# Kernel tuning notes

Hardware: AMD Instinct MI355X
Metric: run time of the kernel (lower is better)

The kernel has to match this reference:

```python
import jax, jax.numpy as jnp
import numpy as np

B, S, T, E, H = 16, 96, 50, 128, 128
D2 = 2 * H
V = 32000
NGRAM = 2
ALPHA = 0.25


def _lstm(x, Wih, Whh, b, reverse=False):
    # x: [N, T, E] -> outputs [N, T, H], final h, c (PyTorch gate order i,f,g,o)
    xt = jnp.swapaxes(x, 0, 1)
    if reverse:
        xt = xt[::-1]
    n = x.shape[0]
    h = Whh.shape[1]
    init = (jnp.zeros((n, h), x.dtype), jnp.zeros((n, h), x.dtype))

    def step(carry, xin):
        hprev, cprev = carry
        g = xin @ Wih.T + hprev @ Whh.T + b
        i, f, gg, o = jnp.split(g, 4, axis=-1)
        c = jax.nn.sigmoid(f) * cprev + jax.nn.sigmoid(i) * jnp.tanh(gg)
        hnew = jax.nn.sigmoid(o) * jnp.tanh(c)
        return (hnew, c), hnew

    (hT, cT), outs = jax.lax.scan(step, init, xt)
    if reverse:
        outs = outs[::-1]
    return jnp.swapaxes(outs, 0, 1), hT, cT


def _gru(x, h, Wi, Wh, bi, bh):
    # PyTorch GRUCell, gate order r,z,n
    gi = x @ Wi.T + bi
    gh = h @ Wh.T + bh
    ir, iz, inn = jnp.split(gi, 3, axis=-1)
    hr, hz, hn = jnp.split(gh, 3, axis=-1)
    r = jax.nn.sigmoid(ir + hr)
    z = jax.nn.sigmoid(iz + hz)
    n = jnp.tanh(inn + r * hn)
    return (1.0 - z) * n + z * h


def _norm_scale(x):
    # (||x|| + alpha) / (||x|| + 1), detached as in the original
    v = jnp.linalg.norm(x, axis=1)
    return jax.lax.stop_gradient(((v + ALPHA) / (v + 1.0))[:, None])


def setup_inputs() -> dict:
    key = jax.random.key(0)
    ks = jax.random.split(key, 30)
    rn = lambda k, sh: jax.random.normal(k, sh, jnp.float32) * 0.05
    return {
        "enc_batch": jax.random.randint(ks[0], (B * S, T), 0, V),
        "struct_parent": jax.random.randint(ks[1], (B, S, S), 0, B * S + 1),
        "struct_child": jax.random.randint(ks[2], (B, S, S), 0, B * S + 1),
        "mask_emb": (jax.random.uniform(ks[3], (B, S, S, 1)) < 0.2).astype(jnp.float32),
        "emb_table": rn(ks[4], (V, E)),
        "Wih_f": rn(ks[5], (4 * H, E)), "Whh_f": rn(ks[6], (4 * H, H)), "b_f": rn(ks[7], (4 * H,)),
        "Wih_b": rn(ks[8], (4 * H, E)), "Whh_b": rn(ks[9], (4 * H, H)), "b_b": rn(ks[10], (4 * H,)),
        "Wc": rn(ks[11], (H, D2)), "bc": rn(ks[12], (H,)),
        "Whr": rn(ks[13], (H, D2)), "bhr": rn(ks[14], (H,)),
        "Wi_cp": rn(ks[15], (3 * D2, D2)), "Wh_cp": rn(ks[16], (3 * D2, D2)),
        "bi_cp": rn(ks[17], (3 * D2,)), "bh_cp": rn(ks[18], (3 * D2,)),
        "Wi_pc": rn(ks[19], (3 * D2, D2)), "Wh_pc": rn(ks[20], (3 * D2, D2)),
        "bi_pc": rn(ks[21], (3 * D2,)), "bh_pc": rn(ks[22], (3 * D2,)),
    }


def reference(enc_batch, struct_parent, struct_child, mask_emb, emb_table,
              Wih_f, Whh_f, b_f, Wih_b, Whh_b, b_b, Wc, bc, Whr, bhr,
              Wi_cp, Wh_cp, bi_cp, bh_cp, Wi_pc, Wh_pc, bi_pc, bh_pc):
    # Sentence encoder (bidirectional LSTM); dropout=0 -> identity
    emb = emb_table[enc_batch]                       # [B*S, T, E]
    _, hf, cf = _lstm(emb, Wih_f, Whh_f, b_f)
    _, hb, cb = _lstm(emb, Wih_b, Whh_b, b_b, reverse=True)
    c_red = jax.nn.relu(jnp.concatenate([cf, cb], 1) @ Wc.T + bc)
    h_red = jax.nn.relu(jnp.concatenate([hf, hb], 1) @ Whr.T + bhr)
    enc_states = jnp.concatenate([c_red, h_red], 1)  # [B*S, 2H]
    zero = jnp.zeros((1, D2), enc_states.dtype)
    hidden = jnp.concatenate([zero, enc_states], 0)  # [B*S+1, 2H]; row 0 = zero_emb

    # child -> parent message passing
    for _ in range(NGRAM):
        p = hidden[struct_parent].reshape(-1, D2)    # gather [B*S*S, 2H]
        c = hidden[struct_child].reshape(-1, D2)
        ch = _gru(c, p, Wi_cp, Wh_cp, bi_cp, bh_cp).reshape(B, S, S, D2)
        ch = (ch * mask_emb).sum(1).reshape(B * S, D2)
        ch = jnp.concatenate([zero, ch], 0)
        hidden = hidden + ch * _norm_scale(ch)

    # parent -> child message passing
    for _ in range(NGRAM):
        p = hidden[struct_parent].reshape(-1, D2)
        c = hidden[struct_child].reshape(-1, D2)
        ch = _gru(p, c, Wi_pc, Wh_pc, bi_pc, bh_pc).reshape(B, S, S, D2)
        ch = (ch * mask_emb).sum(2).reshape(B * S, D2)
        ch = jnp.concatenate([zero, ch], 0)
        hidden = hidden + ch * _norm_scale(ch)

    return hidden
```

## Files before the change

### kernel.cpp

```cpp
#include <hip/hip_runtime.h>

typedef unsigned short u16;
typedef __attribute__((ext_vector_type(8))) short bf8;
typedef __attribute__((ext_vector_type(4))) short s16x4;
typedef __attribute__((ext_vector_type(4))) float f32x4;
typedef __attribute__((ext_vector_type(4))) int   i32x4;

#define S_   96
#define T_   50
#define NSEQ 1536
#define NR   1537
#define XROW 520

__device__ __forceinline__ float bf2f(u16 u){ return __uint_as_float(((unsigned)u)<<16); }
__device__ __forceinline__ u16 f2bf(float f){
  unsigned u = __float_as_uint(f);
  u += 0x7fffu + ((u>>16)&1u);
  return (u16)(u>>16);
}
__device__ __forceinline__ float sigm(float x){
  return __builtin_amdgcn_rcpf(1.f + __expf(-x));
}
__device__ __forceinline__ float tanh_(float x){
  return 1.f - 2.f*__builtin_amdgcn_rcpf(__expf(2.f*x) + 1.f);
}
__device__ __forceinline__ void bar_lds(){
  asm volatile("s_waitcnt lgkmcnt(0)\n\ts_barrier" ::: "memory");
}

struct CvtArgs { const float* s[10]; u16* d[10]; };
__global__ __launch_bounds__(256) void prep_kernel(CvtArgs a,
    const int* __restrict__ par, const int* __restrict__ chi,
    const float* __restrict__ mask,
    int2* __restrict__ ent0, int* __restrict__ cnt0,
    int2* __restrict__ ent1, int* __restrict__ cnt1)
{
  if (blockIdx.x < 1088){
    int e = (blockIdx.x*256 + threadIdx.x)*4;
    if (e >= 1114112) return;
    int t, off;
    if (e < 262144){ t = e>>16; off = e & 65535; }
    else if (e < 327680){ int e2=e-262144; t = 4+(e2>>15); off = e2&32767; }
    else { int e3=e-327680; t = 6 + e3/196608; off = e3%196608; }
    int src = off;
    if (t < 4){
      int colp = off>>7, k = off&127;
      int orig = ((colp>>4)&3)*128 + ((colp>>6)<<4) + (colp&15);
      src = orig*128 + k;
    }
    f32x4 v = *reinterpret_cast<const f32x4*>(a.s[t]+src);
    s16x4 o;
    #pragma unroll
    for (int i=0;i<4;i++) o[i]=(short)f2bf(v[i]);
    *reinterpret_cast<s16x4*>(a.d[t]+off) = o;
  } else {
    const int rr = blockIdx.x - 1088;
    __shared__ int c0s, c1s;
    if (threadIdx.x==0){ c0s=0; c1s=0; }
    __syncthreads();
    const int l = threadIdx.x;
    if (l < S_){
      const int b = rr/S_, fx = rr%S_, base = b*S_*S_;
      int idx = base + l*S_ + fx;
      if (mask[idx] != 0.f){
        int p = atomicAdd(&c0s, 1);
        ent0[rr*S_ + p] = make_int2(chi[idx], par[idx]);
      }
      int jdx = base + fx*S_ + l;
      if (mask[jdx] != 0.f){
        int p = atomicAdd(&c1s, 1);
        ent1[rr*S_ + p] = make_int2(par[jdx], chi[jdx]);
      }
    }
    __syncthreads();
    if (threadIdx.x==0){ cnt0[rr]=c0s; cnt1[rr]=c1s; }
  }
}

__global__ __launch_bounds__(512, 2) void lstm_kernel(
    const int* __restrict__ enc, const float* __restrict__ emb,
    const u16* __restrict__ WihF, const u16* __restrict__ WhhF, const float* __restrict__ bF,
    const u16* __restrict__ WihB, const u16* __restrict__ WhhB, const float* __restrict__ bB,
    u16* __restrict__ c_cat, u16* __restrict__ h_cat)
{
  __shared__ short xh[16*XROW];
  __shared__ int   toks[16*T_];

  const int tid  = threadIdx.x;
  const int wave = tid>>6;
  const int lane = tid&63;
  const int dir  = blockIdx.y;
  const int s0   = blockIdx.x*16;

  const u16* Wih = dir ? WihB : WihF;
  const u16* Whh = dir ? WhhB : WhhF;
  const float* bb = dir ? bB  : bF;

  for (int i=tid; i<16*T_; i+=512)
    toks[i] = enc[(s0 + i/T_)*T_ + (i%T_)];

  const int mL   = lane&15;
  const int quad = lane>>4;
  const int kb   = quad*8;

  bf8 Breg[4][8];
  f32x4 bias4[4];
  #pragma unroll
  for (int n=0;n<4;n++){
    int colp = wave*64 + n*16 + mL;
    bias4[n] = *reinterpret_cast<const f32x4*>(bb + n*128 + wave*16 + quad*4);
    #pragma unroll
    for (int ks=0;ks<8;ks++){
      int k = ks*32 + kb;
      const u16* p = (k<128) ? (Wih + colp*128 + k) : (Whh + colp*128 + (k-128));
      Breg[n][ks] = *reinterpret_cast<const bf8*>(p);
      asm volatile("" : "+v"(Breg[n][ks]));
    }
  }

  if (tid<256){
    int r = tid>>4, c = tid&15;
    *reinterpret_cast<i32x4*>(&xh[r*XROW + 256 + c*8]) = (i32x4){0,0,0,0};
  }

  const int srow = tid>>5, schunk = tid&31;
  float cst[4] = {0.f,0.f,0.f,0.f};
  float hst[4] = {0.f,0.f,0.f,0.f};

  __syncthreads();

  {
    int tok = toks[srow*T_ + (dir ? (T_-1) : 0)];
    f32x4 xv = *reinterpret_cast<const f32x4*>(emb + tok*128 + schunk*4);
    s16x4 xp;
    #pragma unroll
    for (int i=0;i<4;i++) xp[i]=(short)f2bf(xv[i]);
    *reinterpret_cast<s16x4*>(&xh[srow*XROW + schunk*4]) = xp;
  }
  f32x4 xv1, xv2;
  {
    int tok1 = toks[srow*T_ + (dir ? (T_-2) : 1)];
    xv1 = *reinterpret_cast<const f32x4*>(emb + tok1*128 + schunk*4);
    int tok2 = toks[srow*T_ + (dir ? (T_-3) : 2)];
    xv2 = *reinterpret_cast<const f32x4*>(emb + tok2*128 + schunk*4);
  }
  __syncthreads();

  for (int t=0;t<T_;t++){
    const int cb = t&1, nb2 = (t+1)&1;
    if (t+1 < T_){
      s16x4 xp;
      #pragma unroll
      for (int i=0;i<4;i++) xp[i]=(short)f2bf(xv1[i]);
      *reinterpret_cast<s16x4*>(&xh[srow*XROW + nb2*128 + schunk*4]) = xp;
    }
    xv1 = xv2;
    if (t+3 < T_){
      int tok = toks[srow*T_ + (dir ? (T_-4-t) : (t+3))];
      xv2 = *reinterpret_cast<const f32x4*>(emb + tok*128 + schunk*4);
    }

    f32x4 acc[4];
    #pragma unroll
    for (int i=0;i<4;i++) acc[i] = (f32x4){0.f,0.f,0.f,0.f};
    #pragma unroll
    for (int ks=0;ks<8;ks++){
      int k = ks*32 + kb;
      int off = (k<128) ? (cb*128 + k) : (256 + cb*128 + (k-128));
      bf8 b = *reinterpret_cast<const bf8*>(&xh[mL*XROW + off]);
      #pragma unroll
      for (int n=0;n<4;n++)
        acc[n] = __builtin_amdgcn_mfma_f32_16x16x32_bf16(Breg[n][ks], b, acc[n], 0,0,0);
    }

    s16x4 hp;
    #pragma unroll
    for (int i=0;i<4;i++){
      float gi_ = acc[0][i]+bias4[0][i];
      float gf_ = acc[1][i]+bias4[1][i];
      float gg_ = acc[2][i]+bias4[2][i];
      float go_ = acc[3][i]+bias4[3][i];
      float c = sigm(gf_)*cst[i] + sigm(gi_)*tanh_(gg_);
      float h = sigm(go_)*tanh_(c);
      cst[i]=c; hst[i]=h;
      hp[i] = (short)f2bf(h);
    }
    *reinterpret_cast<s16x4*>(&xh[mL*XROW + 256 + nb2*128 + wave*16 + quad*4]) = hp;
    bar_lds();
  }

  {
    const int ch = wave*16 + quad*4;
    const int gs = s0 + mL;
    s16x4 cp_, hp_;
    #pragma unroll
    for (int i=0;i<4;i++){ cp_[i]=(short)f2bf(cst[i]); hp_[i]=(short)f2bf(hst[i]); }
    *reinterpret_cast<s16x4*>(c_cat + gs*256 + dir*128 + ch) = cp_;
    *reinterpret_cast<s16x4*>(h_cat + gs*256 + dir*128 + ch) = hp_;
  }
}

__global__ __launch_bounds__(256) void reduce_kernel(
    const u16* __restrict__ c_cat, const u16* __restrict__ h_cat,
    const u16* __restrict__ Wc, const float* __restrict__ bc,
    const u16* __restrict__ Whr, const float* __restrict__ bhr,
    float* __restrict__ hidf, u16* __restrict__ hidb)
{
  const int tid=threadIdx.x, wave=tid>>6, lane=tid&63;
  const int mL=lane&15, quad=lane>>4, kb=quad*8;
  const int m0 = blockIdx.x*64;
  const u16* A    = (wave<2) ? c_cat : h_cat;
  const u16* W    = (wave<2) ? Wc  : Whr;
  const float* bv = (wave<2) ? bc  : bhr;
  const int nb    = (wave&1)*64;
  const int obase = (wave<2) ? 0 : 128;

  f32x4 acc[4][4];
  #pragma unroll
  for (int mt=0;mt<4;mt++)
    #pragma unroll
    for (int nt=0;nt<4;nt++) acc[mt][nt] = (f32x4){0.f,0.f,0.f,0.f};

  #pragma unroll
  for (int ks=0;ks<8;ks++){
    int k = ks*32 + kb;
    bf8 bfr[4];
    #pragma unroll
    for (int nt=0;nt<4;nt++)
      bfr[nt] = *reinterpret_cast<const bf8*>(W + (nb+nt*16+mL)*256 + k);
    #pragma unroll
    for (int mt=0;mt<4;mt++){
      bf8 a = *reinterpret_cast<const bf8*>(A + (m0+mt*16+mL)*256 + k);
      #pragma unroll
      for (int nt=0;nt<4;nt++)
        acc[mt][nt] = __builtin_amdgcn_mfma_f32_16x16x32_bf16(a, bfr[nt], acc[mt][nt], 0,0,0);
    }
  }
  const int row0 = quad*4;
  float biasv[4];
  #pragma unroll
  for (int nt=0;nt<4;nt++) biasv[nt] = bv[nb+nt*16+mL];
  #pragma unroll
  for (int mt=0;mt<4;mt++){
    #pragma unroll
    for (int nt=0;nt<4;nt++){
      int col = obase + nb + nt*16 + mL;
      #pragma unroll
      for (int i=0;i<4;i++){
        int r = m0 + mt*16 + row0 + i;
        float v = fmaxf(acc[mt][nt][i] + biasv[nt], 0.f);
        hidf[(r+1)*256 + col] = v;
        hidb[(r+1)*256 + col] = f2bf(v);
      }
    }
  }
  if (blockIdx.x==0 && tid<64){
    #pragma unroll
    for (int j=0;j<4;j++){ hidf[tid*4+j] = 0.f; hidb[tid*4+j] = 0; }
  }
}

__global__ __launch_bounds__(256) void gates_gemm_kernel(
    const u16* __restrict__ hidb,
    const u16* __restrict__ Wi, const u16* __restrict__ Wh,
    const float* __restrict__ bi, const float* __restrict__ bh,
    u16* __restrict__ gi, u16* __restrict__ gh)
{
  const int tid=threadIdx.x, wave=tid>>6, lane=tid&63;
  const int mL=lane&15, quad=lane>>4, kb=quad*8;
  const int m0 = blockIdx.x*32;
  const int n0 = blockIdx.y*256 + wave*64;
  const bool isI = (n0 < 768);
  const u16* W    = isI ? Wi : Wh;
  const float* bv = isI ? bi : bh;
  u16* out        = isI ? gi : gh;
  const int nbc   = isI ? n0 : (n0-768);

  int arow[2];
  #pragma unroll
  for (int mt=0;mt<2;mt++) arow[mt] = min(m0+mt*16+mL, NR-1);

  f32x4 acc[2][4];
  #pragma unroll
  for (int mt=0;mt<2;mt++)
    #pragma unroll
    for (int nt=0;nt<4;nt++) acc[mt][nt] = (f32x4){0.f,0.f,0.f,0.f};

  #pragma unroll
  for (int ks=0;ks<8;ks++){
    int k = ks*32 + kb;
    bf8 bfr[4];
    #pragma unroll
    for (int nt=0;nt<4;nt++)
      bfr[nt] = *reinterpret_cast<const bf8*>(W + (nbc+nt*16+mL)*256 + k);
    #pragma unroll
    for (int mt=0;mt<2;mt++){
      bf8 a = *reinterpret_cast<const bf8*>(hidb + arow[mt]*256 + k);
      #pragma unroll
      for (int nt=0;nt<4;nt++)
        acc[mt][nt] = __builtin_amdgcn_mfma_f32_16x16x32_bf16(a, bfr[nt], acc[mt][nt], 0,0,0);
    }
  }
  const int row0 = quad*4;
  float biasv[4];
  #pragma unroll
  for (int nt=0;nt<4;nt++) biasv[nt] = bv[nbc+nt*16+mL];
  #pragma unroll
  for (int mt=0;mt<2;mt++){
    #pragma unroll
    for (int nt=0;nt<4;nt++){
      #pragma unroll
      for (int i=0;i<4;i++){
        int r = m0 + mt*16 + row0 + i;
        if (r < NR)
          out[r*768 + nbc + nt*16 + mL] = f2bf(acc[mt][nt][i] + biasv[nt]);
      }
    }
  }
}

__global__ __launch_bounds__(512) void pair_kernel(
    const u16* __restrict__ gi, const u16* __restrict__ gh,
    const float* __restrict__ hin,
    float* __restrict__ hout, u16* __restrict__ bout, float* __restrict__ dout,
    const int2* __restrict__ ent, const int* __restrict__ cnt)
{
  const int r = blockIdx.x;
  const int tid = threadIdx.x, wave = tid>>6, lane = tid&63;
  __shared__ float part[8][260];
  __shared__ float ssum[4];
  if (r==0){
    if (tid<256){
      hout[tid]=0.f; bout[tid]=0;
      if (dout) dout[tid]=0.f;
    }
    return;
  }
  const int rr = r-1;
  const int n  = cnt[rr];
  const int2* e = ent + rr*S_;
  const int ch0 = lane*4;

  float a0=0.f, a1=0.f, a2=0.f, a3=0.f;
  for (int k=wave; k<n; k+=8){
    int2 pr = e[k];
    const u16* gx = gi + pr.x*768 + ch0;
    const u16* gy = gh + pr.y*768 + ch0;
    s16x4 vi0 = *reinterpret_cast<const s16x4*>(gx);
    s16x4 vi1 = *reinterpret_cast<const s16x4*>(gx+256);
    s16x4 vi2 = *reinterpret_cast<const s16x4*>(gx+512);
    s16x4 vh0 = *reinterpret_cast<const s16x4*>(gy);
    s16x4 vh1 = *reinterpret_cast<const s16x4*>(gy+256);
    s16x4 vh2 = *reinterpret_cast<const s16x4*>(gy+512);
    f32x4 hv  = *reinterpret_cast<const f32x4*>(hin + pr.y*256 + ch0);
    float o[4];
    #pragma unroll
    for (int i=0;i<4;i++){
      float rg = sigm(bf2f((u16)vi0[i]) + bf2f((u16)vh0[i]));
      float zg = sigm(bf2f((u16)vi1[i]) + bf2f((u16)vh1[i]));
      float ng = tanh_(bf2f((u16)vi2[i]) + rg*bf2f((u16)vh2[i]));
      o[i] = (1.f-zg)*ng + zg*hv[i];
    }
    a0 += o[0]; a1 += o[1]; a2 += o[2]; a3 += o[3];
  }
  *reinterpret_cast<f32x4*>(&part[wave][ch0]) = (f32x4){a0,a1,a2,a3};
  __syncthreads();

  if (tid < 256){
    float tot = part[0][tid] + part[1][tid] + part[2][tid] + part[3][tid]
              + part[4][tid] + part[5][tid] + part[6][tid] + part[7][tid];
    part[0][tid] = tot;
    float sq = tot*tot;
    #pragma unroll
    for (int off=32; off>0; off>>=1) sq += __shfl_xor(sq, off, 64);
    if (lane==0) ssum[wave] = sq;
  }
  __syncthreads();
  if (tid < 256){
    float tot = part[0][tid];
    float v  = sqrtf(ssum[0]+ssum[1]+ssum[2]+ssum[3]);
    float sc = (v + 0.25f)*__builtin_amdgcn_rcpf(v + 1.f);
    float nv = hin[r*256 + tid] + tot*sc;
    hout[r*256 + tid] = nv;
    bout[r*256 + tid] = f2bf(nv);
    if (dout) dout[r*256 + tid] = nv;
  }
}

extern "C" void kernel_launch(void* const* d_in, const int* in_sizes, int n_in,
                              void* d_out, int out_size, void* d_ws, size_t ws_size,
                              hipStream_t stream)
{
  const int*   enc  = (const int*)  d_in[0];
  const int*   spar = (const int*)  d_in[1];
  const int*   schi = (const int*)  d_in[2];
  const float* mask = (const float*)d_in[3];
  const float* emb  = (const float*)d_in[4];
  const float* WihF = (const float*)d_in[5];
  const float* WhhF = (const float*)d_in[6];
  const float* bF   = (const float*)d_in[7];
  const float* WihB = (const float*)d_in[8];
  const float* WhhB = (const float*)d_in[9];
  const float* bB   = (const float*)d_in[10];
  const float* Wc   = (const float*)d_in[11];
  const float* bc   = (const float*)d_in[12];
  const float* Whr  = (const float*)d_in[13];
  const float* bhr  = (const float*)d_in[14];
  const float* WiCP = (const float*)d_in[15];
  const float* WhCP = (const float*)d_in[16];
  const float* biCP = (const float*)d_in[17];
  const float* bhCP = (const float*)d_in[18];
  const float* WiPC = (const float*)d_in[19];
  const float* WhPC = (const float*)d_in[20];
  const float* biPC = (const float*)d_in[21];
  const float* bhPC = (const float*)d_in[22];

  char* ws = (char*)d_ws;
  u16*   c_cat = (u16*)  (ws + 0);
  u16*   h_cat = (u16*)  (ws + 786432);
  float* hf0   = (float*)(ws + 1572864);
  float* hf1   = (float*)(ws + 3146752);
  u16*   hb    = (u16*)  (ws + 4720640);
  u16*   gi    = (u16*)  (ws + 5507584);
  u16*   gh    = (u16*)  (ws + 7868416);
  u16*   wbf   = (u16*)  (ws + 10229248);
  int2*  ent0  = (int2*) (ws + 12457472);
  int2*  ent1  = (int2*) (ws + 13637120);
  int*   cnt0  = (int*)  (ws + 14816768);
  int*   cnt1  = (int*)  (ws + 14822912);
  float* out   = (float*)d_out;

  u16* bWihF = wbf + 0;
  u16* bWhhF = wbf + 65536;
  u16* bWihB = wbf + 131072;
  u16* bWhhB = wbf + 196608;
  u16* bWc   = wbf + 262144;
  u16* bWhr  = wbf + 294912;
  u16* bWiCP = wbf + 327680;
  u16* bWhCP = wbf + 524288;
  u16* bWiPC = wbf + 720896;
  u16* bWhPC = wbf + 917504;

  CvtArgs ca;
  ca.s[0]=WihF; ca.s[1]=WhhF; ca.s[2]=WihB; ca.s[3]=WhhB;
  ca.s[4]=Wc;   ca.s[5]=Whr;
  ca.s[6]=WiCP; ca.s[7]=WhCP; ca.s[8]=WiPC; ca.s[9]=WhPC;
  ca.d[0]=bWihF; ca.d[1]=bWhhF; ca.d[2]=bWihB; ca.d[3]=bWhhB;
  ca.d[4]=bWc;   ca.d[5]=bWhr;
  ca.d[6]=bWiCP; ca.d[7]=bWhCP; ca.d[8]=bWiPC; ca.d[9]=bWhPC;
  prep_kernel<<<dim3(1088+NSEQ), dim3(256), 0, stream>>>(
      ca, spar, schi, mask, ent0, cnt0, ent1, cnt1);

  lstm_kernel<<<dim3(96,2), dim3(512), 0, stream>>>(
      enc, emb, bWihF,bWhhF,bF, bWihB,bWhhB,bB, c_cat, h_cat);
  reduce_kernel<<<dim3(24), dim3(256), 0, stream>>>(
      c_cat,h_cat, bWc,bc,bWhr,bhr, hf0,hb);

  float* hfb[2] = {hf0,hf1};
  int cur = 0;
  for (int it=0; it<4; it++){
    const u16* Wi   = (it<2)?bWiCP:bWiPC;
    const u16* Wh   = (it<2)?bWhCP:bWhPC;
    const float* bi = (it<2)?biCP:biPC;
    const float* bh = (it<2)?bhCP:bhPC;
    int nxt = cur^1;
    gates_gemm_kernel<<<dim3(49,6), dim3(256), 0, stream>>>(
        hb, Wi,Wh,bi,bh, gi,gh);
    pair_kernel<<<dim3(NR), dim3(512), 0, stream>>>(
        gi,gh, hfb[cur], hfb[nxt], hb,
        (it==3)?out:(float*)nullptr,
        (it<2)?ent0:ent1, (it<2)?cnt0:cnt1);
    cur = nxt;
  }
}
```

Baseline: 325.9 us.

## Assign one wave per output row in pair kernel, drop LDS reduction

Rewrites pair_kernel so that each 64-lane wave handles a whole output row, with four rows per 256-thread block. The previous version spread each row's entries across eight waves and combined them through shared memory with two block barriers. Entry indices are now loaded once per lane and broadcast with shuffles, and the norm is reduced inside the wave only. This removes LDS traffic and barriers, but each wave now walks all of a row's entries serially, giving less parallelism per row and longer dependent chains when rows have many entries. Rows with more than 96 entries are not covered by the index preload.

```diff
diff --git a/kernel.cpp b/kernel.cpp
--- a/kernel.cpp
+++ b/kernel.cpp
@@ -319,40 +319,44 @@
   }
 }
 
-__global__ __launch_bounds__(512) void pair_kernel(
+__global__ __launch_bounds__(256) void pair_kernel(
     const u16* __restrict__ gi, const u16* __restrict__ gh,
     const float* __restrict__ hin,
     float* __restrict__ hout, u16* __restrict__ bout, float* __restrict__ dout,
     const int2* __restrict__ ent, const int* __restrict__ cnt)
 {
-  const int r = blockIdx.x;
-  const int tid = threadIdx.x, wave = tid>>6, lane = tid&63;
-  __shared__ float part[8][260];
-  __shared__ float ssum[4];
-  if (r==0){
-    if (tid<256){
-      hout[tid]=0.f; bout[tid]=0;
-      if (dout) dout[tid]=0.f;
-    }
+  const int row  = blockIdx.x*4 + (threadIdx.x>>6);
+  const int lane = threadIdx.x & 63;
+  if (row >= NR) return;
+  const int ch0 = lane*4;
+  if (row == 0){
+    f32x4 z = {0.f,0.f,0.f,0.f};
+    s16x4 zb = {0,0,0,0};
+    *reinterpret_cast<f32x4*>(hout + ch0) = z;
+    *reinterpret_cast<s16x4*>(bout + ch0) = zb;
+    if (dout) *reinterpret_cast<f32x4*>(dout + ch0) = z;
     return;
   }
-  const int rr = r-1;
+  const int rr = row - 1;
   const int n  = cnt[rr];
   const int2* e = ent + rr*S_;
-  const int ch0 = lane*4;
+  int2 eA = e[lane];
+  int2 eB = (n > 64) ? e[64 + (lane & 31)] : eA;
 
   float a0=0.f, a1=0.f, a2=0.f, a3=0.f;
-  for (int k=wave; k<n; k+=8){
-    int2 pr = e[k];
-    const u16* gx = gi + pr.x*768 + ch0;
-    const u16* gy = gh + pr.y*768 + ch0;
+  for (int k=0; k<n; k++){
+    int xr, hr;
+    if (k < 64){ xr = __shfl(eA.x, k, 64);    hr = __shfl(eA.y, k, 64); }
+    else       { xr = __shfl(eB.x, k-64, 64); hr = __shfl(eB.y, k-64, 64); }
+    const u16* gx = gi + xr*768 + ch0;
+    const u16* gy = gh + hr*768 + ch0;
     s16x4 vi0 = *reinterpret_cast<const s16x4*>(gx);
     s16x4 vi1 = *reinterpret_cast<const s16x4*>(gx+256);
     s16x4 vi2 = *reinterpret_cast<const s16x4*>(gx+512);
     s16x4 vh0 = *reinterpret_cast<const s16x4*>(gy);
     s16x4 vh1 = *reinterpret_cast<const s16x4*>(gy+256);
     s16x4 vh2 = *reinterpret_cast<const s16x4*>(gy+512);
-    f32x4 hv  = *reinterpret_cast<const f32x4*>(hin + pr.y*256 + ch0);
+    f32x4 hv  = *reinterpret_cast<const f32x4*>(hin + hr*256 + ch0);
     float o[4];
     #pragma unroll
     for (int i=0;i<4;i++){
@@ -363,28 +367,21 @@
     }
     a0 += o[0]; a1 += o[1]; a2 += o[2]; a3 += o[3];
   }
-  *reinterpret_cast<f32x4*>(&part[wave][ch0]) = (f32x4){a0,a1,a2,a3};
-  __syncthreads();
-
-  if (tid < 256){
-    float tot = part[0][tid] + part[1][tid] + part[2][tid] + part[3][tid]
-              + part[4][tid] + part[5][tid] + part[6][tid] + part[7][tid];
-    part[0][tid] = tot;
-    float sq = tot*tot;
-    #pragma unroll
-    for (int off=32; off>0; off>>=1) sq += __shfl_xor(sq, off, 64);
-    if (lane==0) ssum[wave] = sq;
-  }
-  __syncthreads();
-  if (tid < 256){
-    float tot = part[0][tid];
-    float v  = sqrtf(ssum[0]+ssum[1]+ssum[2]+ssum[3]);
-    float sc = (v + 0.25f)*__builtin_amdgcn_rcpf(v + 1.f);
-    float nv = hin[r*256 + tid] + tot*sc;
-    hout[r*256 + tid] = nv;
-    bout[r*256 + tid] = f2bf(nv);
-    if (dout) dout[r*256 + tid] = nv;
-  }
+
+  float sq = a0*a0 + a1*a1 + a2*a2 + a3*a3;
+  #pragma unroll
+  for (int off=32; off>0; off>>=1) sq += __shfl_xor(sq, off, 64);
+  float v  = sqrtf(sq);
+  float sc = (v + 0.25f)*__builtin_amdgcn_rcpf(v + 1.f);
+
+  f32x4 hv = *reinterpret_cast<const f32x4*>(hin + row*256 + ch0);
+  f32x4 nv = { hv[0]+a0*sc, hv[1]+a1*sc, hv[2]+a2*sc, hv[3]+a3*sc };
+  *reinterpret_cast<f32x4*>(hout + row*256 + ch0) = nv;
+  s16x4 nb;
+  #pragma unroll
+  for (int i=0;i<4;i++) nb[i] = (short)f2bf(nv[i]);
+  *reinterpret_cast<s16x4*>(bout + row*256 + ch0) = nb;
+  if (dout) *reinterpret_cast<f32x4*>(dout + row*256 + ch0) = nv;
 }
 
 extern "C" void kernel_launch(void* const* d_in, const int* in_sizes, int n_in,
@@ -466,7 +463,7 @@
     int nxt = cur^1;
     gates_gemm_kernel<<<dim3(49,6), dim3(256), 0, stream>>>(
         hb, Wi,Wh,bi,bh, gi,gh);
-    pair_kernel<<<dim3(NR), dim3(512), 0, stream>>>(
+    pair_kernel<<<dim3((NR+3)/4), dim3(256), 0, stream>>>(
         gi,gh, hfb[cur], hfb[nxt], hb,
         (it==3)?out:(float*)nullptr,
         (it<2)?ent0:ent1, (it<2)?cnt0:cnt1);
```

Result: slower. 352.2 us (+8.1%).

## Software-pipeline pair-kernel gathers with zero-row padding and halve GEMM M-tile

Applied to the files above, without the earlier changes.

The pair kernel now prefetches the next entry's gate and hidden rows while computing the current one, which hides gather latency. To let it do that safely, each parent's entry list is padded to a multiple of four with a dedicated zero sentinel row (index 1537). The prep kernel zero-fills that row in the gi, gh and hidden buffers, and the workspace offsets shift to make room for it. Separately, the gates GEMM uses 16-row tiles instead of 32, doubling the grid for more parallelism at the cost of re-reading the weights more often. The padded entries also add wasted GRU evaluations on the zero row, though the GRU of an all-zero row is zero, so the sums stay correct.

```diff
diff --git a/kernel.cpp b/kernel.cpp
--- a/kernel.cpp
+++ b/kernel.cpp
@@ -10,6 +10,7 @@
 #define T_   50
 #define NSEQ 1536
 #define NR   1537
+#define ZR   1537
 #define XROW 520
 
 __device__ __forceinline__ float bf2f(u16 u){ return __uint_as_float(((unsigned)u)<<16); }
@@ -33,7 +34,9 @@
     const int* __restrict__ par, const int* __restrict__ chi,
     const float* __restrict__ mask,
     int2* __restrict__ ent0, int* __restrict__ cnt0,
-    int2* __restrict__ ent1, int* __restrict__ cnt1)
+    int2* __restrict__ ent1, int* __restrict__ cnt1,
+    u16* __restrict__ gi, u16* __restrict__ gh,
+    float* __restrict__ hf0, float* __restrict__ hf1)
 {
   if (blockIdx.x < 1088){
     int e = (blockIdx.x*256 + threadIdx.x)*4;
@@ -53,7 +56,7 @@
     #pragma unroll
     for (int i=0;i<4;i++) o[i]=(short)f2bf(v[i]);
     *reinterpret_cast<s16x4*>(a.d[t]+off) = o;
-  } else {
+  } else if (blockIdx.x < 1088 + NSEQ){
     const int rr = blockIdx.x - 1088;
     __shared__ int c0s, c1s;
     if (threadIdx.x==0){ c0s=0; c1s=0; }
@@ -73,7 +76,15 @@
       }
     }
     __syncthreads();
-    if (threadIdx.x==0){ cnt0[rr]=c0s; cnt1[rr]=c1s; }
+    const int c0 = c0s, c1 = c1s;
+    const int c0p = (c0+3)&~3, c1p = (c1+3)&~3;
+    if (l >= c0 && l < c0p) ent0[rr*S_ + l] = make_int2(ZR, ZR);
+    if (l >= c1 && l < c1p) ent1[rr*S_ + l] = make_int2(ZR, ZR);
+    if (threadIdx.x==0){ cnt0[rr]=c0p; cnt1[rr]=c1p; }
+  } else {
+    const int l = threadIdx.x;
+    for (int i=l; i<768; i+=256){ gi[ZR*768+i]=0; gh[ZR*768+i]=0; }
+    if (l < 256){ hf0[ZR*256+l]=0.f; hf1[ZR*256+l]=0.f; }
   }
 }
 
@@ -268,7 +279,7 @@
 {
   const int tid=threadIdx.x, wave=tid>>6, lane=tid&63;
   const int mL=lane&15, quad=lane>>4, kb=quad*8;
-  const int m0 = blockIdx.x*32;
+  const int m0 = blockIdx.x*16;
   const int n0 = blockIdx.y*256 + wave*64;
   const bool isI = (n0 < 768);
   const u16* W    = isI ? Wi : Wh;
@@ -276,15 +287,11 @@
   u16* out        = isI ? gi : gh;
   const int nbc   = isI ? n0 : (n0-768);
 
-  int arow[2];
-  #pragma unroll
-  for (int mt=0;mt<2;mt++) arow[mt] = min(m0+mt*16+mL, NR-1);
-
-  f32x4 acc[2][4];
-  #pragma unroll
-  for (int mt=0;mt<2;mt++)
-    #pragma unroll
-    for (int nt=0;nt<4;nt++) acc[mt][nt] = (f32x4){0.f,0.f,0.f,0.f};
+  const int arow = min(m0+mL, NR-1);
+
+  f32x4 acc[4];
+  #pragma unroll
+  for (int nt=0;nt<4;nt++) acc[nt] = (f32x4){0.f,0.f,0.f,0.f};
 
   #pragma unroll
   for (int ks=0;ks<8;ks++){
@@ -293,28 +300,20 @@
     #pragma unroll
     for (int nt=0;nt<4;nt++)
       bfr[nt] = *reinterpret_cast<const bf8*>(W + (nbc+nt*16+mL)*256 + k);
-    #pragma unroll
-    for (int mt=0;mt<2;mt++){
-      bf8 a = *reinterpret_cast<const bf8*>(hidb + arow[mt]*256 + k);
-      #pragma unroll
-      for (int nt=0;nt<4;nt++)
-        acc[mt][nt] = __builtin_amdgcn_mfma_f32_16x16x32_bf16(a, bfr[nt], acc[mt][nt], 0,0,0);
-    }
+    bf8 a = *reinterpret_cast<const bf8*>(hidb + arow*256 + k);
+    #pragma unroll
+    for (int nt=0;nt<4;nt++)
+      acc[nt] = __builtin_amdgcn_mfma_f32_16x16x32_bf16(a, bfr[nt], acc[nt], 0,0,0);
   }
   const int row0 = quad*4;
-  float biasv[4];
-  #pragma unroll
-  for (int nt=0;nt<4;nt++) biasv[nt] = bv[nbc+nt*16+mL];
-  #pragma unroll
-  for (int mt=0;mt<2;mt++){
-    #pragma unroll
-    for (int nt=0;nt<4;nt++){
-      #pragma unroll
-      for (int i=0;i<4;i++){
-        int r = m0 + mt*16 + row0 + i;
-        if (r < NR)
-          out[r*768 + nbc + nt*16 + mL] = f2bf(acc[mt][nt][i] + biasv[nt]);
-      }
+  #pragma unroll
+  for (int nt=0;nt<4;nt++){
+    float biasv = bv[nbc+nt*16+mL];
+    #pragma unroll
+    for (int i=0;i<4;i++){
+      int r = m0 + row0 + i;
+      if (r < NR)
+        out[r*768 + nbc + nt*16 + mL] = f2bf(acc[nt][i] + biasv);
     }
   }
 }
@@ -342,26 +341,44 @@
   const int ch0 = lane*4;
 
   float a0=0.f, a1=0.f, a2=0.f, a3=0.f;
-  for (int k=wave; k<n; k+=8){
-    int2 pr = e[k];
-    const u16* gx = gi + pr.x*768 + ch0;
-    const u16* gy = gh + pr.y*768 + ch0;
+  int k = wave;
+  if (k < n){
+    int2 E = e[k];
+    const u16* gx = gi + E.x*768 + ch0;
+    const u16* gy = gh + E.y*768 + ch0;
     s16x4 vi0 = *reinterpret_cast<const s16x4*>(gx);
     s16x4 vi1 = *reinterpret_cast<const s16x4*>(gx+256);
     s16x4 vi2 = *reinterpret_cast<const s16x4*>(gx+512);
     s16x4 vh0 = *reinterpret_cast<const s16x4*>(gy);
     s16x4 vh1 = *reinterpret_cast<const s16x4*>(gy+256);
     s16x4 vh2 = *reinterpret_cast<const s16x4*>(gy+512);
-    f32x4 hv  = *reinterpret_cast<const f32x4*>(hin + pr.y*256 + ch0);
-    float o[4];
-    #pragma unroll
-    for (int i=0;i<4;i++){
-      float rg = sigm(bf2f((u16)vi0[i]) + bf2f((u16)vh0[i]));
-      float zg = sigm(bf2f((u16)vi1[i]) + bf2f((u16)vh1[i]));
-      float ng = tanh_(bf2f((u16)vi2[i]) + rg*bf2f((u16)vh2[i]));
-      o[i] = (1.f-zg)*ng + zg*hv[i];
-    }
-    a0 += o[0]; a1 += o[1]; a2 += o[2]; a3 += o[3];
+    f32x4 hv  = *reinterpret_cast<const f32x4*>(hin + E.y*256 + ch0);
+    while (true){
+      const int k2 = k + 8;
+      const bool more = (k2 < n);
+      const int kc = more ? k2 : k;
+      int2 E2 = e[kc];
+      const u16* gx2 = gi + E2.x*768 + ch0;
+      const u16* gy2 = gh + E2.y*768 + ch0;
+      s16x4 wi0 = *reinterpret_cast<const s16x4*>(gx2);
+      s16x4 wi1 = *reinterpret_cast<const s16x4*>(gx2+256);
+      s16x4 wi2 = *reinterpret_cast<const s16x4*>(gx2+512);
+      s16x4 wh0 = *reinterpret_cast<const s16x4*>(gy2);
+      s16x4 wh1 = *reinterpret_cast<const s16x4*>(gy2+256);
+      s16x4 wh2 = *reinterpret_cast<const s16x4*>(gy2+512);
+      f32x4 hv2 = *reinterpret_cast<const f32x4*>(hin + E2.y*256 + ch0);
+      #pragma unroll
+      for (int i=0;i<4;i++){
+        float rg = sigm(bf2f((u16)vi0[i]) + bf2f((u16)vh0[i]));
+        float zg = sigm(bf2f((u16)vi1[i]) + bf2f((u16)vh1[i]));
+        float ng = tanh_(bf2f((u16)vi2[i]) + rg*bf2f((u16)vh2[i]));
+        float o  = (1.f-zg)*ng + zg*hv[i];
+        if (i==0) a0 += o; else if (i==1) a1 += o; else if (i==2) a2 += o; else a3 += o;
+      }
+      if (!more) break;
+      vi0=wi0; vi1=wi1; vi2=wi2; vh0=wh0; vh1=wh1; vh2=wh2; hv=hv2;
+      k = k2;
+    }
   }
   *reinterpret_cast<f32x4*>(&part[wave][ch0]) = (f32x4){a0,a1,a2,a3};
   __syncthreads();
@@ -419,15 +436,15 @@
   u16*   c_cat = (u16*)  (ws + 0);
   u16*   h_cat = (u16*)  (ws + 786432);
   float* hf0   = (float*)(ws + 1572864);
-  float* hf1   = (float*)(ws + 3146752);
-  u16*   hb    = (u16*)  (ws + 4720640);
-  u16*   gi    = (u16*)  (ws + 5507584);
-  u16*   gh    = (u16*)  (ws + 7868416);
-  u16*   wbf   = (u16*)  (ws + 10229248);
-  int2*  ent0  = (int2*) (ws + 12457472);
-  int2*  ent1  = (int2*) (ws + 13637120);
-  int*   cnt0  = (int*)  (ws + 14816768);
-  int*   cnt1  = (int*)  (ws + 14822912);
+  float* hf1   = (float*)(ws + 3148800);
+  u16*   hb    = (u16*)  (ws + 4724736);
+  u16*   gi    = (u16*)  (ws + 5511680);
+  u16*   gh    = (u16*)  (ws + 7874048);
+  u16*   wbf   = (u16*)  (ws + 10236416);
+  int2*  ent0  = (int2*) (ws + 12464640);
+  int2*  ent1  = (int2*) (ws + 13644288);
+  int*   cnt0  = (int*)  (ws + 14823936);
+  int*   cnt1  = (int*)  (ws + 14830080);
   float* out   = (float*)d_out;
 
   u16* bWihF = wbf + 0;
@@ -448,8 +465,8 @@
   ca.d[0]=bWihF; ca.d[1]=bWhhF; ca.d[2]=bWihB; ca.d[3]=bWhhB;
   ca.d[4]=bWc;   ca.d[5]=bWhr;
   ca.d[6]=bWiCP; ca.d[7]=bWhCP; ca.d[8]=bWiPC; ca.d[9]=bWhPC;
-  prep_kernel<<<dim3(1088+NSEQ), dim3(256), 0, stream>>>(
-      ca, spar, schi, mask, ent0, cnt0, ent1, cnt1);
+  prep_kernel<<<dim3(1088+NSEQ+1), dim3(256), 0, stream>>>(
+      ca, spar, schi, mask, ent0, cnt0, ent1, cnt1, gi, gh, hf0, hf1);
 
   lstm_kernel<<<dim3(96,2), dim3(512), 0, stream>>>(
       enc, emb, bWihF,bWhhF,bF, bWihB,bWhhB,bB, c_cat, h_cat);
@@ -464,7 +481,7 @@
     const float* bi = (it<2)?biCP:biPC;
     const float* bh = (it<2)?bhCP:bhPC;
     int nxt = cur^1;
-    gates_gemm_kernel<<<dim3(49,6), dim3(256), 0, stream>>>(
+    gates_gemm_kernel<<<dim3(97,6), dim3(256), 0, stream>>>(
         hb, Wi,Wh,bi,bh, gi,gh);
     pair_kernel<<<dim3(NR), dim3(512), 0, stream>>>(
         gi,gh, hfb[cur], hfb[nxt], hb,
```

New measurement: 332.2 us. No clear change (+1.9%).
